# Kernel tuning notes

Hardware: AMD Instinct MI355X
Metric: run time of the kernel (lower is better)

The kernel has to match this reference:

```python
import jax, jax.numpy as jnp
import numpy as np

N_WITHIN = 20   # n_labels for active dataset (cityscapes)
N_CROSS = 27    # n_labels for other dataset (idd)
ALPHA = 0.5
BETA = 0.5
T = 1.0


def _l2norm_rows(w):
    return w / jnp.sqrt(jnp.sum(w * w, axis=1, keepdims=True) + 1e-12)


def setup_inputs() -> dict:
    key = jax.random.key(0)
    k1, k2, k3, k4 = jax.random.split(key, 4)
    B, D, H, W = 4, 64, 512, 512
    encoder_op = jax.random.normal(k1, (B, D, H, W), jnp.float32)
    # conv weights are row-normalized label embeddings (frozen in original)
    w_within = _l2norm_rows(jax.random.normal(k2, (N_WITHIN, D), jnp.float32))
    w_cross = _l2norm_rows(jax.random.normal(k3, (N_CROSS, D), jnp.float32))
    targets = jax.random.randint(k4, (B, H, W), 0, N_WITHIN, dtype=jnp.int32)
    return {"encoder_op": encoder_op, "w_within": w_within,
            "w_cross": w_cross, "targets": targets}


def _entropy_loss(logits):
    # mean over (b,h,w) of -sum_c p * log p, softmax over channel dim 1
    logp = jax.nn.log_softmax(logits, axis=1)
    p = jnp.exp(logp)
    return jnp.mean(-jnp.sum(p * logp, axis=1)).reshape(-1)


def reference(encoder_op, w_within, w_cross, targets):
    # 1x1 conv == channel contraction; drop last (background) channel as in torch code
    within_map = jnp.einsum('bdhw,nd->bnhw', encoder_op, w_within)[:, :-1]
    cross_map = jnp.einsum('bdhw,nd->bnhw', encoder_op, w_cross)[:, :-1] / T
    loss_unsup = ALPHA * _entropy_loss(cross_map) + BETA * _entropy_loss(within_map)

    # _update_centroids: per-label masked sum == segment_sum over flattened pixels
    B, D, H, W = encoder_op.shape
    feats = encoder_op.transpose(0, 2, 3, 1).reshape(-1, D)  # [B*H*W, D]
    labs = targets.reshape(-1)                               # [B*H*W]
    centroids = jax.ops.segment_sum(feats, labs, num_segments=N_WITHIN)  # [N, D]
    counts = jax.ops.segment_sum(jnp.ones_like(labs, dtype=jnp.int32), labs,
                                 num_segments=N_WITHIN)                   # [N]
    # original detaches centroids (.data)
    return loss_unsup, jax.lax.stop_gradient(centroids), counts
```

## Files before the change

### kernel.cpp

```cpp
#include <hip/hip_runtime.h>
#include <hip/hip_bf16.h>

#define HW_   (512 * 512)
#define B_    4
#define D_    64
#define NPIX  (B_ * HW_)
#define NW    19
#define NC    26
#define NLAB  (NW + NC)
#define NSEG  20
#define THREADS 256
#define TILE  THREADS

#define LW(X)  X(0)X(1)X(2)X(3)X(4)X(5)X(6)X(7)X(8)X(9)X(10)X(11)X(12)X(13)X(14)X(15)X(16)X(17)X(18)
#define LWR(X) X(1)X(2)X(3)X(4)X(5)X(6)X(7)X(8)X(9)X(10)X(11)X(12)X(13)X(14)X(15)X(16)X(17)X(18)
#define LC(X)  X(19)X(20)X(21)X(22)X(23)X(24)X(25)X(26)X(27)X(28)X(29)X(30)X(31)X(32)X(33)X(34)X(35)X(36)X(37)X(38)X(39)X(40)X(41)X(42)X(43)X(44)
#define LCR(X) X(20)X(21)X(22)X(23)X(24)X(25)X(26)X(27)X(28)X(29)X(30)X(31)X(32)X(33)X(34)X(35)X(36)X(37)X(38)X(39)X(40)X(41)X(42)X(43)X(44)
#define LA(X)  LW(X) LC(X)

__global__ __launch_bounds__(THREADS, 4)
void fused_embed(const float* __restrict__ enc, const float* __restrict__ wW,
                 const float* __restrict__ wC, const int* __restrict__ targ,
                 float* __restrict__ out)
{
    __shared__ float sCent[NSEG][D_ + 1];
    __shared__ int   sCount[NSEG];
    __shared__ float sRed[THREADS / 64];

    const int tid = threadIdx.x;

    for (int i = tid; i < NSEG * (D_ + 1); i += THREADS) (&sCent[0][0])[i] = 0.f;
    if (tid < NSEG) sCount[tid] = 0;
    __syncthreads();

    const int p   = blockIdx.x * TILE + tid;
    const int b   = (blockIdx.x * TILE) / HW_;
    const int hw0 = p - b * HW_;
    const float* fp = enc + (size_t)b * (D_ * HW_) + hw0;
    const int lab = targ[p];

#define DECL_ACC(n) float a##n = 0.f;
    LA(DECL_ACC)

#define WPTR(n) (((n) < NW) ? (wW + (n) * D_) : (wC + ((n) - NW) * D_))

#pragma unroll 2
    for (int dc = 0; dc < D_ / 4; ++dc) {
        const float* fpc = fp + (size_t)dc * 4 * HW_;
        float f0 = fpc[0];
        float f1 = fpc[HW_];
        float f2 = fpc[2 * HW_];
        float f3 = fpc[3 * HW_];

        atomicAdd(&sCent[lab][dc * 4 + 0], f0);
        atomicAdd(&sCent[lab][dc * 4 + 1], f1);
        atomicAdd(&sCent[lab][dc * 4 + 2], f2);
        atomicAdd(&sCent[lab][dc * 4 + 3], f3);

#define FMA_ACC(n) { const float4 w = *(const float4*)(WPTR(n) + dc * 4); \
                     a##n = fmaf(w.w, f3, fmaf(w.z, f2, fmaf(w.y, f1, fmaf(w.x, f0, a##n)))); }
        LA(FMA_ACC)
#undef FMA_ACC
    }

    atomicAdd(&sCount[lab], 1);

    float lossAcc = 0.f;
    {
        float m = a0;
#define MX(n) m = fmaxf(m, a##n);
        LWR(MX)
#undef MX
        float S = 0.f, Wt = 0.f;
#define ES(n) { float s = a##n - m; float e = __expf(s); S += e; Wt = fmaf(e, s, Wt); }
        LW(ES)
#undef ES
        lossAcc += __logf(S) - Wt / S;
    }
    {
        float m = a19;
#define MX(n) m = fmaxf(m, a##n);
        LCR(MX)
#undef MX
        float S = 0.f, Wt = 0.f;
#define ES(n) { float s = a##n - m; float e = __expf(s); S += e; Wt = fmaf(e, s, Wt); }
        LC(ES)
#undef ES
        lossAcc += __logf(S) - Wt / S;
    }

#pragma unroll
    for (int off = 32; off; off >>= 1) lossAcc += __shfl_down(lossAcc, off);
    if ((tid & 63) == 0) sRed[tid >> 6] = lossAcc;
    __syncthreads();
    if (tid == 0) {
        float s = 0.f;
#pragma unroll
        for (int w = 0; w < THREADS / 64; ++w) s += sRed[w];
        atomicAdd(out, s * (0.5f / (float)NPIX));
    }

    for (int i = tid; i < NSEG * D_; i += THREADS) {
        int n = i >> 6, d = i & 63;
        atomicAdd(&out[1 + i], sCent[n][d]);
    }
    if (tid < NSEG) atomicAdd(&out[1 + NSEG * D_ + tid], (float)sCount[tid]);
}

extern "C" void kernel_launch(void* const* d_in, const int* in_sizes, int n_in,
                              void* d_out, int out_size, void* d_ws, size_t ws_size,
                              hipStream_t stream) {
    const float* enc = (const float*)d_in[0];
    const float* wW  = (const float*)d_in[1];
    const float* wC  = (const float*)d_in[2];
    const int*   targ = (const int*)d_in[3];
    float* out = (float*)d_out;

    hipMemsetAsync(d_out, 0, (size_t)out_size * sizeof(float), stream);

    fused_embed<<<dim3(NPIX / TILE), dim3(THREADS), 0, stream>>>(enc, wW, wC, targ, out);
}
```

Before: 380.1 us.

## Swap loop order: hold pixel features in registers, stream labels with online softmax

The kernel now loads all 64 feature values of each pixel into registers up front. It then loops over labels one at a time, computing each dot product and folding it into an online max/sum/weighted-sum entropy accumulator, instead of keeping 45 label accumulators live across the feature loop. This exchanges 45 live accumulators for 64 live feature registers. It also adds two extra exps per label for the online rescaling, and moves all centroid shared-memory atomics before the dot products. Register pressure and the extra exp work may change occupancy and ALU cost.

```diff
diff --git a/kernel.cpp b/kernel.cpp
--- a/kernel.cpp
+++ b/kernel.cpp
@@ -7,16 +7,24 @@
 #define NPIX  (B_ * HW_)
 #define NW    19
 #define NC    26
-#define NLAB  (NW + NC)
 #define NSEG  20
 #define THREADS 256
 #define TILE  THREADS
 
-#define LW(X)  X(0)X(1)X(2)X(3)X(4)X(5)X(6)X(7)X(8)X(9)X(10)X(11)X(12)X(13)X(14)X(15)X(16)X(17)X(18)
-#define LWR(X) X(1)X(2)X(3)X(4)X(5)X(6)X(7)X(8)X(9)X(10)X(11)X(12)X(13)X(14)X(15)X(16)X(17)X(18)
-#define LC(X)  X(19)X(20)X(21)X(22)X(23)X(24)X(25)X(26)X(27)X(28)X(29)X(30)X(31)X(32)X(33)X(34)X(35)X(36)X(37)X(38)X(39)X(40)X(41)X(42)X(43)X(44)
-#define LCR(X) X(20)X(21)X(22)X(23)X(24)X(25)X(26)X(27)X(28)X(29)X(30)X(31)X(32)X(33)X(34)X(35)X(36)X(37)X(38)X(39)X(40)X(41)X(42)X(43)X(44)
-#define LA(X)  LW(X) LC(X)
+#define FOREACH_CHUNK(X) \
+  X(0,0,f0,f1,f2,f3)      X(1,1,f4,f5,f6,f7)      X(2,2,f8,f9,f10,f11)     X(3,3,f12,f13,f14,f15) \
+  X(4,0,f16,f17,f18,f19)  X(5,1,f20,f21,f22,f23)  X(6,2,f24,f25,f26,f27)   X(7,3,f28,f29,f30,f31) \
+  X(8,0,f32,f33,f34,f35)  X(9,1,f36,f37,f38,f39)  X(10,2,f40,f41,f42,f43)  X(11,3,f44,f45,f46,f47) \
+  X(12,0,f48,f49,f50,f51) X(13,1,f52,f53,f54,f55) X(14,2,f56,f57,f58,f59)  X(15,3,f60,f61,f62,f63)
+
+#define ONLINE(m, S, W, a) { \
+    float mN = fmaxf(m, a); \
+    float c0 = __expf(m - mN); \
+    float s0 = (a) - mN; \
+    float e0 = __expf(s0); \
+    W = fmaf(m - mN, S, W) * c0 + s0 * e0; \
+    S = fmaf(S, c0, e0); \
+    m = mN; }
 
 __global__ __launch_bounds__(THREADS, 4)
 void fused_embed(const float* __restrict__ enc, const float* __restrict__ wW,
@@ -39,55 +47,50 @@
     const float* fp = enc + (size_t)b * (D_ * HW_) + hw0;
     const int lab = targ[p];
 
-#define DECL_ACC(n) float a##n = 0.f;
-    LA(DECL_ACC)
+#define LOADC(c, k, fa, fb, fc2, fd) \
+    float fa = fp[(4*(c)+0) * HW_]; \
+    float fb = fp[(4*(c)+1) * HW_]; \
+    float fc2 = fp[(4*(c)+2) * HW_]; \
+    float fd = fp[(4*(c)+3) * HW_];
+    FOREACH_CHUNK(LOADC)
+#undef LOADC
 
-#define WPTR(n) (((n) < NW) ? (wW + (n) * D_) : (wC + ((n) - NW) * D_))
+#define ATOMC(c, k, fa, fb, fc2, fd) \
+    atomicAdd(&sCent[lab][4*(c)+0], fa); \
+    atomicAdd(&sCent[lab][4*(c)+1], fb); \
+    atomicAdd(&sCent[lab][4*(c)+2], fc2); \
+    atomicAdd(&sCent[lab][4*(c)+3], fd);
+    FOREACH_CHUNK(ATOMC)
+#undef ATOMC
+    atomicAdd(&sCount[lab], 1);
 
-#pragma unroll 2
-    for (int dc = 0; dc < D_ / 4; ++dc) {
-        const float* fpc = fp + (size_t)dc * 4 * HW_;
-        float f0 = fpc[0];
-        float f1 = fpc[HW_];
-        float f2 = fpc[2 * HW_];
-        float f3 = fpc[3 * HW_];
+#define DOTC(c, k, fa, fb, fc2, fd) { \
+    const float4 w = *(const float4*)(wr + 4*(c)); \
+    d##k = fmaf(w.x, fa, d##k); d##k = fmaf(w.y, fb, d##k); \
+    d##k = fmaf(w.z, fc2, d##k); d##k = fmaf(w.w, fd, d##k); }
 
-        atomicAdd(&sCent[lab][dc * 4 + 0], f0);
-        atomicAdd(&sCent[lab][dc * 4 + 1], f1);
-        atomicAdd(&sCent[lab][dc * 4 + 2], f2);
-        atomicAdd(&sCent[lab][dc * 4 + 3], f3);
-
-#define FMA_ACC(n) { const float4 w = *(const float4*)(WPTR(n) + dc * 4); \
-                     a##n = fmaf(w.w, f3, fmaf(w.z, f2, fmaf(w.y, f1, fmaf(w.x, f0, a##n)))); }
-        LA(FMA_ACC)
-#undef FMA_ACC
+    float mW = -1e30f, SW = 0.f, WWt = 0.f;
+#pragma unroll 1
+    for (int n = 0; n < NW; ++n) {
+        const float* wr = wW + n * D_;
+        float d0 = 0.f, d1 = 0.f, d2 = 0.f, d3 = 0.f;
+        FOREACH_CHUNK(DOTC)
+        float a = (d0 + d1) + (d2 + d3);
+        ONLINE(mW, SW, WWt, a)
     }
 
-    atomicAdd(&sCount[lab], 1);
+    float mC = -1e30f, SC = 0.f, WCt = 0.f;
+#pragma unroll 1
+    for (int n = 0; n < NC; ++n) {
+        const float* wr = wC + n * D_;
+        float d0 = 0.f, d1 = 0.f, d2 = 0.f, d3 = 0.f;
+        FOREACH_CHUNK(DOTC)
+        float a = (d0 + d1) + (d2 + d3);
+        ONLINE(mC, SC, WCt, a)
+    }
+#undef DOTC
 
-    float lossAcc = 0.f;
-    {
-        float m = a0;
-#define MX(n) m = fmaxf(m, a##n);
-        LWR(MX)
-#undef MX
-        float S = 0.f, Wt = 0.f;
-#define ES(n) { float s = a##n - m; float e = __expf(s); S += e; Wt = fmaf(e, s, Wt); }
-        LW(ES)
-#undef ES
-        lossAcc += __logf(S) - Wt / S;
-    }
-    {
-        float m = a19;
-#define MX(n) m = fmaxf(m, a##n);
-        LCR(MX)
-#undef MX
-        float S = 0.f, Wt = 0.f;
-#define ES(n) { float s = a##n - m; float e = __expf(s); S += e; Wt = fmaf(e, s, Wt); }
-        LC(ES)
-#undef ES
-        lossAcc += __logf(S) - Wt / S;
-    }
+    float lossAcc = (__logf(SW) - WWt / SW) + (__logf(SC) - WCt / SC);
 
 #pragma unroll
     for (int off = 32; off; off >>= 1) lossAcc += __shfl_down(lossAcc, off);
```

Result: no change. 384.9 us (+1.3%).

## Transpose weights to channel-major and stream one channel per iteration

Applied to the files above, without the earlier changes.

Adds a small kernel that transposes both weight matrices into a channel-major padded buffer in workspace, so the main loop reads one contiguous weight row per input channel. The main loop processes one channel at a time with a one-step prefetch and no unrolling, the occupancy target is set via waves_per_eu, and the softmax max-subtraction is removed. The aim is to cut the instruction and register cost of the weight loads and reduction. Skipping the max subtraction risks overflow if logits are large.

```diff
diff --git a/kernel.cpp b/kernel.cpp
--- a/kernel.cpp
+++ b/kernel.cpp
@@ -7,83 +7,79 @@
 #define NPIX  (B_ * HW_)
 #define NW    19
 #define NC    26
-#define NLAB  (NW + NC)
+#define NLAB  45
 #define NSEG  20
+#define WSTRIDE 48
 #define THREADS 256
-#define TILE  THREADS
 
 #define LW(X)  X(0)X(1)X(2)X(3)X(4)X(5)X(6)X(7)X(8)X(9)X(10)X(11)X(12)X(13)X(14)X(15)X(16)X(17)X(18)
-#define LWR(X) X(1)X(2)X(3)X(4)X(5)X(6)X(7)X(8)X(9)X(10)X(11)X(12)X(13)X(14)X(15)X(16)X(17)X(18)
 #define LC(X)  X(19)X(20)X(21)X(22)X(23)X(24)X(25)X(26)X(27)X(28)X(29)X(30)X(31)X(32)X(33)X(34)X(35)X(36)X(37)X(38)X(39)X(40)X(41)X(42)X(43)X(44)
-#define LCR(X) X(20)X(21)X(22)X(23)X(24)X(25)X(26)X(27)X(28)X(29)X(30)X(31)X(32)X(33)X(34)X(35)X(36)X(37)X(38)X(39)X(40)X(41)X(42)X(43)X(44)
 #define LA(X)  LW(X) LC(X)
 
-__global__ __launch_bounds__(THREADS, 4)
-void fused_embed(const float* __restrict__ enc, const float* __restrict__ wW,
-                 const float* __restrict__ wC, const int* __restrict__ targ,
-                 float* __restrict__ out)
+__global__ void transpose_w(const float* __restrict__ wW, const float* __restrict__ wC,
+                            float* __restrict__ wT) {
+    int i = blockIdx.x * 256 + threadIdx.x;
+    if (i < D_ * NLAB) {
+        int c = i / NLAB, n = i - c * NLAB;
+        wT[c * WSTRIDE + n] = (n < NW) ? wW[n * D_ + c] : wC[(n - NW) * D_ + c];
+    }
+}
+
+__global__ __launch_bounds__(THREADS)
+__attribute__((amdgpu_waves_per_eu(6, 6)))
+void fused_embed(const float* __restrict__ enc, const float* __restrict__ wT,
+                 const int* __restrict__ targ, float* __restrict__ out)
 {
     __shared__ float sCent[NSEG][D_ + 1];
     __shared__ int   sCount[NSEG];
     __shared__ float sRed[THREADS / 64];
 
     const int tid = threadIdx.x;
-
     for (int i = tid; i < NSEG * (D_ + 1); i += THREADS) (&sCent[0][0])[i] = 0.f;
     if (tid < NSEG) sCount[tid] = 0;
     __syncthreads();
 
-    const int p   = blockIdx.x * TILE + tid;
-    const int b   = (blockIdx.x * TILE) / HW_;
+    const int p   = blockIdx.x * THREADS + tid;
+    const int b   = (blockIdx.x * THREADS) / HW_;
     const int hw0 = p - b * HW_;
     const float* fp = enc + (size_t)b * (D_ * HW_) + hw0;
     const int lab = targ[p];
 
 #define DECL_ACC(n) float a##n = 0.f;
     LA(DECL_ACC)
+#undef DECL_ACC
 
-#define WPTR(n) (((n) < NW) ? (wW + (n) * D_) : (wC + ((n) - NW) * D_))
-
-#pragma unroll 2
-    for (int dc = 0; dc < D_ / 4; ++dc) {
-        const float* fpc = fp + (size_t)dc * 4 * HW_;
-        float f0 = fpc[0];
-        float f1 = fpc[HW_];
-        float f2 = fpc[2 * HW_];
-        float f3 = fpc[3 * HW_];
-
-        atomicAdd(&sCent[lab][dc * 4 + 0], f0);
-        atomicAdd(&sCent[lab][dc * 4 + 1], f1);
-        atomicAdd(&sCent[lab][dc * 4 + 2], f2);
-        atomicAdd(&sCent[lab][dc * 4 + 3], f3);
-
-#define FMA_ACC(n) { const float4 w = *(const float4*)(WPTR(n) + dc * 4); \
-                     a##n = fmaf(w.w, f3, fmaf(w.z, f2, fmaf(w.y, f1, fmaf(w.x, f0, a##n)))); }
-        LA(FMA_ACC)
-#undef FMA_ACC
+    float fcur = fp[0];
+#pragma unroll 1
+    for (int c = 0; c < D_ - 1; ++c) {
+        float fnext = fp[(size_t)(c + 1) * HW_];
+        const float* wr = wT + c * WSTRIDE;
+#define FMA1(n) a##n = fmaf(fcur, wr[n], a##n);
+        LA(FMA1)
+#undef FMA1
+        atomicAdd(&sCent[lab][c], fcur);
+        fcur = fnext;
     }
-
+    {
+        const float* wr = wT + (D_ - 1) * WSTRIDE;
+#define FMA1(n) a##n = fmaf(fcur, wr[n], a##n);
+        LA(FMA1)
+#undef FMA1
+        atomicAdd(&sCent[lab][D_ - 1], fcur);
+    }
     atomicAdd(&sCount[lab], 1);
 
-    float lossAcc = 0.f;
+    float lossAcc;
     {
-        float m = a0;
-#define MX(n) m = fmaxf(m, a##n);
-        LWR(MX)
-#undef MX
         float S = 0.f, Wt = 0.f;
-#define ES(n) { float s = a##n - m; float e = __expf(s); S += e; Wt = fmaf(e, s, Wt); }
+#define ES(n) { float e = __expf(a##n); S += e; Wt = fmaf(e, a##n, Wt); }
         LW(ES)
 #undef ES
-        lossAcc += __logf(S) - Wt / S;
+        lossAcc = __logf(S) - Wt / S;
     }
     {
-        float m = a19;
-#define MX(n) m = fmaxf(m, a##n);
-        LCR(MX)
-#undef MX
         float S = 0.f, Wt = 0.f;
-#define ES(n) { float s = a##n - m; float e = __expf(s); S += e; Wt = fmaf(e, s, Wt); }
+#define ES(n) { float e = __expf(a##n); S += e; Wt = fmaf(e, a##n, Wt); }
         LC(ES)
 #undef ES
         lossAcc += __logf(S) - Wt / S;
@@ -115,8 +111,10 @@
     const float* wC  = (const float*)d_in[2];
     const int*   targ = (const int*)d_in[3];
     float* out = (float*)d_out;
+    float* wT  = (float*)d_ws;
 
     hipMemsetAsync(d_out, 0, (size_t)out_size * sizeof(float), stream);
 
-    fused_embed<<<dim3(NPIX / TILE), dim3(THREADS), 0, stream>>>(enc, wW, wC, targ, out);
+    transpose_w<<<dim3((D_ * NLAB + 255) / 256), dim3(256), 0, stream>>>(wW, wC, wT);
+    fused_embed<<<dim3(NPIX / THREADS), dim3(THREADS), 0, stream>>>(enc, wT, targ, out);
 }
```

Result: slower. 444.0 us (+16.8%).
